# Performance work log

Measured on AMD Instinct MI355X. Metric: run time of the kernel, lower is better.

The kernel has to match this reference:

```python
import jax, jax.numpy as jnp
import numpy as np

N_NODES = 100000
N_EDGES = 3200000
IN_CH = 128
HID = 64
N_CLASSES = 10


def setup_inputs() -> dict:
    key = jax.random.key(0)
    ks = jax.random.split(key, 12)
    def lin(kw, kb, fan_in, fan_out):
        bound = 1.0 / np.sqrt(fan_in)
        W = jax.random.uniform(kw, (fan_in, fan_out), jnp.float32, -bound, bound)
        b = jax.random.uniform(kb, (fan_out,), jnp.float32, -bound, bound)
        return W, b
    x = jax.random.normal(ks[0], (N_NODES, IN_CH), jnp.float32)
    edge_index = jax.random.randint(ks[1], (2, N_EDGES), 0, N_NODES, jnp.int32)
    W1a, b1a = lin(ks[2], ks[3], IN_CH, HID)
    W2a, b2a = lin(ks[4], ks[5], HID, HID)
    W1b, b1b = lin(ks[6], ks[7], HID, HID)
    W2b, b2b = lin(ks[8], ks[9], HID, HID)
    Wl, bl = lin(ks[10], ks[11], HID, N_CLASSES)
    return {"x": x, "edge_index": edge_index,
            "W1a": W1a, "b1a": b1a, "W2a": W2a, "b2a": b2a,
            "W1b": W1b, "b1b": b1b, "W2b": W2b, "b2b": b2b,
            "Wl": Wl, "bl": bl}


def gin_conv(x, src, dst, W1, b1, W2, b2):
    # sum-aggregate neighbor messages: agg[i] = sum_{(src->i)} x[src]
    agg = jax.ops.segment_sum(x[src], dst, num_segments=N_NODES)
    h = agg + x  # (1 + eps) * x with eps = 0 (GINConv default)
    h = jnp.maximum(h @ W1 + b1, 0.0)  # Linear -> ReLU
    return h @ W2 + b2                 # Linear


def reference(x, edge_index, W1a, b1a, W2a, b2a, W1b, b1b, W2b, b2b, Wl, bl):
    src, dst = edge_index[0], edge_index[1]
    h = gin_conv(x, src, dst, W1a, b1a, W2a, b2a)
    h = jnp.maximum(h, 0.0)
    h = gin_conv(h, src, dst, W1b, b1b, W2b, b2b)
    h = jnp.maximum(h, 0.0)
    logits = h @ Wl + bl
    return jax.nn.log_softmax(logits, axis=1)
```

## Files before the change

### kernel.cpp

```cpp
#include <hip/hip_runtime.h>
#include <hip/hip_bf16.h>

#define N_NODES 100000
#define N_EDGES 3200000
#define IN_CH 128
#define HID 64
#define N_CLASSES 10
#define NTILES 6250

#define NB 391
#define NPB 256
#define BCAP 10240
#define CHUNK 8192

typedef unsigned short u16;
typedef unsigned int u32;

typedef __attribute__((ext_vector_type(8))) short bf16x8;
typedef __attribute__((ext_vector_type(4))) float f32x4;

static __device__ __forceinline__ float u2f(u32 u) {
    union { u32 i; float f; } v; v.i = u; return v.f;
}
static __device__ __forceinline__ u16 f2bf(float f) {
    __hip_bfloat16 b = __float2bfloat16(f);
    return *(u16*)&b;
}
static __device__ __forceinline__ u32 pack2(float lo, float hi) {
    return (u32)f2bf(lo) | ((u32)f2bf(hi) << 16);
}


__global__ void __launch_bounds__(1024) passA_k(
        const int* __restrict__ src, const int* __restrict__ dst,
        int* __restrict__ bcnt, u32* __restrict__ stage) {
    __shared__ int lh[NB];
    __shared__ int lb[NB];
    for (int i = threadIdx.x; i < NB; i += 1024) lh[i] = 0;
    __syncthreads();
    int e0 = blockIdx.x * CHUNK;
#pragma unroll
    for (int k = 0; k < CHUNK / 1024; ++k) {
        int e = e0 + k * 1024 + threadIdx.x;
        if (e < N_EDGES) atomicAdd(&lh[dst[e] >> 8], 1);
    }
    __syncthreads();
    for (int i = threadIdx.x; i < NB; i += 1024) {
        lb[i] = atomicAdd(&bcnt[i], lh[i]);
        lh[i] = 0;
    }
    __syncthreads();
#pragma unroll
    for (int k = 0; k < CHUNK / 1024; ++k) {
        int e = e0 + k * 1024 + threadIdx.x;
        if (e < N_EDGES) {
            int d = dst[e];
            int b = d >> 8;
            int p = lb[b] + atomicAdd(&lh[b], 1);
            if (p < BCAP) stage[(size_t)b * BCAP + p] = ((u32)src[e] << 8) | (u32)(d & 255);
        }
    }
}


__global__ void bscan_k(const int* __restrict__ bcnt, int* __restrict__ bbase,
                        int* __restrict__ off) {
    __shared__ int s[512];
    int tid = threadIdx.x;
    int v = (tid < NB) ? min(bcnt[tid], BCAP) : 0;
    s[tid] = v;
    __syncthreads();
    for (int o = 1; o < 512; o <<= 1) {
        int t = (tid >= o) ? s[tid - o] : 0;
        __syncthreads();
        s[tid] += t;
        __syncthreads();
    }
    if (tid < NB) bbase[tid] = s[tid] - v;
    if (tid == NB - 1) off[N_NODES] = s[tid];
}


__global__ void __launch_bounds__(1024) passB_k(
        const int* __restrict__ bcnt, const int* __restrict__ bbase,
        const u32* __restrict__ stage, int* __restrict__ off,
        int* __restrict__ csr) {
    __shared__ int ldeg[NPB];
    __shared__ int loff[NPB + 1];
    __shared__ int lcur[NPB];
    __shared__ int img[BCAP];
    int b = blockIdx.x;
    int nb = min(bcnt[b], BCAP);
    int base = bbase[b];
    const u32* st = stage + (size_t)b * BCAP;
    int tid = threadIdx.x;
    if (tid < NPB) ldeg[tid] = 0;
    __syncthreads();
    for (int i = tid; i < nb; i += 1024) atomicAdd(&ldeg[st[i] & 255u], 1);
    __syncthreads();
    if (tid < NPB) lcur[tid] = ldeg[tid];
    __syncthreads();
    for (int o = 1; o < NPB; o <<= 1) {
        int t = (tid < NPB && tid >= o) ? lcur[tid - o] : 0;
        __syncthreads();
        if (tid < NPB) lcur[tid] += t;
        __syncthreads();
    }
    if (tid < NPB) loff[tid + 1] = lcur[tid];
    if (tid == 0) loff[0] = 0;
    __syncthreads();
    if (tid < NPB) {
        int gnode = (b << 8) + tid;
        if (gnode < N_NODES) off[gnode] = base + loff[tid];
        lcur[tid] = loff[tid];
    }
    __syncthreads();
    for (int i = tid; i < nb; i += 1024) {
        u32 pr = st[i];
        int p = atomicAdd(&lcur[pr & 255u], 1);
        img[p] = (int)(pr >> 8);
    }
    __syncthreads();
    for (int i = tid; i < nb; i += 1024) csr[base + i] = img[i];
}


__global__ void __launch_bounds__(512) gather_k(
        const u16* __restrict__ tab, const int* __restrict__ off,
        const int* __restrict__ csr, u16* __restrict__ outb) {
    int wid = threadIdx.x >> 6, lane = threadIdx.x & 63;
    int g = lane >> 3, c = lane & 7;
    int coff = c << 4;
    const char* tb = (const char*)tab;
    int gw = blockIdx.x * 8 + wid;
    const int NW = 1024 * 8;
    for (int n = gw; n < N_NODES; n += NW) {
        float a0, a1, a2, a3, a4, a5, a6, a7;
        {
            uint4 dS = *(const uint4*)(tb + (size_t)n * 128 + coff);
            u32 sm = (g == 0) ? 0xffffffffu : 0u;
            dS.x &= sm; dS.y &= sm; dS.z &= sm; dS.w &= sm;
            a0 = u2f(dS.x << 16); a1 = u2f(dS.x & 0xffff0000u);
            a2 = u2f(dS.y << 16); a3 = u2f(dS.y & 0xffff0000u);
            a4 = u2f(dS.z << 16); a5 = u2f(dS.z & 0xffff0000u);
            a6 = u2f(dS.w << 16); a7 = u2f(dS.w & 0xffff0000u);
        }
        int e = off[n], e1 = off[n + 1];
        int nfull = (e1 - e) >> 3;
#pragma unroll 4
        for (int it = 0; it < nfull; ++it) {
            int s = csr[e + g];
            uint4 d = *(const uint4*)(tb + (size_t)s * 128 + coff);
            a0 += u2f(d.x << 16); a1 += u2f(d.x & 0xffff0000u);
            a2 += u2f(d.y << 16); a3 += u2f(d.y & 0xffff0000u);
            a4 += u2f(d.z << 16); a5 += u2f(d.z & 0xffff0000u);
            a6 += u2f(d.w << 16); a7 += u2f(d.w & 0xffff0000u);
            e += 8;
        }
        int rem = e1 - e;
        if (rem > 0) {
            int s = csr[e + min(g, rem - 1)];
            u32 m = (g < rem) ? 0xffffffffu : 0u;
            uint4 d = *(const uint4*)(tb + (size_t)s * 128 + coff);
            d.x &= m; d.y &= m; d.z &= m; d.w &= m;
            a0 += u2f(d.x << 16); a1 += u2f(d.x & 0xffff0000u);
            a2 += u2f(d.y << 16); a3 += u2f(d.y & 0xffff0000u);
            a4 += u2f(d.z << 16); a5 += u2f(d.z & 0xffff0000u);
            a6 += u2f(d.w << 16); a7 += u2f(d.w & 0xffff0000u);
        }
        a0 += __shfl_xor(a0, 8);  a1 += __shfl_xor(a1, 8);  a2 += __shfl_xor(a2, 8);
        a3 += __shfl_xor(a3, 8);  a4 += __shfl_xor(a4, 8);  a5 += __shfl_xor(a5, 8);
        a6 += __shfl_xor(a6, 8);  a7 += __shfl_xor(a7, 8);
        a0 += __shfl_xor(a0, 16); a1 += __shfl_xor(a1, 16); a2 += __shfl_xor(a2, 16);
        a3 += __shfl_xor(a3, 16); a4 += __shfl_xor(a4, 16); a5 += __shfl_xor(a5, 16);
        a6 += __shfl_xor(a6, 16); a7 += __shfl_xor(a7, 16);
        a0 += __shfl_xor(a0, 32); a1 += __shfl_xor(a1, 32); a2 += __shfl_xor(a2, 32);
        a3 += __shfl_xor(a3, 32); a4 += __shfl_xor(a4, 32); a5 += __shfl_xor(a5, 32);
        a6 += __shfl_xor(a6, 32); a7 += __shfl_xor(a7, 32);
        if (g == 0) {
            uint4 pk = make_uint4(pack2(a0, a1), pack2(a2, a3), pack2(a4, a5), pack2(a6, a7));
            *(uint4*)((char*)outb + (size_t)n * 128 + coff) = pk;
        }
    }
}


static __device__ __forceinline__ bf16x8 bfragW(const float* __restrict__ W, int ncols,
                                                int kk, int nt, int lane) {
    int k0 = kk * 32 + ((lane >> 4) << 3);
    int col = nt * 16 + (lane & 15);
    bf16x8 b;
#pragma unroll
    for (int j = 0; j < 8; ++j) b[j] = (short)f2bf(W[(size_t)(k0 + j) * ncols + col]);
    return b;
}

static __device__ __forceinline__ bf16x8 bfragWl(const float* __restrict__ Wl,
                                                 int kk, int lane) {
    int k0 = kk * 32 + ((lane >> 4) << 3);
    int col = lane & 15;
    bf16x8 b;
#pragma unroll
    for (int j = 0; j < 8; ++j)
        b[j] = (col < N_CLASSES) ? (short)f2bf(Wl[(size_t)(k0 + j) * N_CLASSES + col]) : (short)0;
    return b;
}

static __device__ __forceinline__ bf16x8 afragSt(const u16* __restrict__ stw,
                                                 int kk, int lane) {
    const u16* p = stw + (size_t)(lane & 15) * 68 + kk * 32 + ((lane >> 4) << 3);
    uint2 q0 = *(const uint2*)p;
    uint2 q1 = *(const uint2*)(p + 4);
    union { uint2 u[2]; bf16x8 v; } cv;
    cv.u[0] = q0; cv.u[1] = q1;
    return cv.v;
}


__global__ void __launch_bounds__(512) lin1_k(
        const float* __restrict__ x, const float* __restrict__ W1,
        u16* __restrict__ yb) {
    __shared__ u16 st[8][16][68];
    int wid = threadIdx.x >> 6, lane = threadIdx.x & 63;
    bf16x8 B[4][4];
#pragma unroll
    for (int kk = 0; kk < 4; ++kk)
#pragma unroll
        for (int nt = 0; nt < 4; ++nt) B[kk][nt] = bfragW(W1, 64, kk, nt, lane);
    int gw = blockIdx.x * 8 + wid;
    const int NW = 782 * 8;
    for (int t = gw; t < NTILES; t += NW) {
        int n0 = t << 4;
        f32x4 acc0 = {0.f, 0.f, 0.f, 0.f}, acc1 = acc0, acc2 = acc0, acc3 = acc0;
#pragma unroll
        for (int kk = 0; kk < 4; ++kk) {
            const float* xr = x + (size_t)(n0 + (lane & 15)) * IN_CH + kk * 32 + ((lane >> 4) << 3);
            float4 f0 = *(const float4*)xr;
            float4 f1 = *(const float4*)(xr + 4);
            bf16x8 a;
            a[0] = (short)f2bf(f0.x); a[1] = (short)f2bf(f0.y);
            a[2] = (short)f2bf(f0.z); a[3] = (short)f2bf(f0.w);
            a[4] = (short)f2bf(f1.x); a[5] = (short)f2bf(f1.y);
            a[6] = (short)f2bf(f1.z); a[7] = (short)f2bf(f1.w);
            acc0 = __builtin_amdgcn_mfma_f32_16x16x32_bf16(a, B[kk][0], acc0, 0, 0, 0);
            acc1 = __builtin_amdgcn_mfma_f32_16x16x32_bf16(a, B[kk][1], acc1, 0, 0, 0);
            acc2 = __builtin_amdgcn_mfma_f32_16x16x32_bf16(a, B[kk][2], acc2, 0, 0, 0);
            acc3 = __builtin_amdgcn_mfma_f32_16x16x32_bf16(a, B[kk][3], acc3, 0, 0, 0);
        }
        int r0 = (lane >> 4) << 2, cl = lane & 15;
#pragma unroll
        for (int i = 0; i < 4; ++i) {
            st[wid][r0 + i][cl]      = f2bf(acc0[i]);
            st[wid][r0 + i][16 + cl] = f2bf(acc1[i]);
            st[wid][r0 + i][32 + cl] = f2bf(acc2[i]);
            st[wid][r0 + i][48 + cl] = f2bf(acc3[i]);
        }
        __builtin_amdgcn_wave_barrier();
        {
            int row = lane >> 2, seg = lane & 3;
            const u16* sp = &st[wid][row][seg * 16];
            uint2 q0 = *(const uint2*)sp;
            uint2 q1 = *(const uint2*)(sp + 4);
            uint2 q2 = *(const uint2*)(sp + 8);
            uint2 q3 = *(const uint2*)(sp + 12);
            char* op = (char*)yb + (size_t)(n0 + row) * 128 + seg * 32;
            *(uint4*)op = make_uint4(q0.x, q0.y, q1.x, q1.y);
            *(uint4*)(op + 16) = make_uint4(q2.x, q2.y, q3.x, q3.y);
        }
        __builtin_amdgcn_wave_barrier();
    }
}


__global__ void __launch_bounds__(512) mlpA_k(
        const u16* __restrict__ ga, const float* __restrict__ b1,
        const float* __restrict__ W2, const float* __restrict__ b2,
        u16* __restrict__ h1b) {
    __shared__ u16 st[8][16][68];
    int wid = threadIdx.x >> 6, lane = threadIdx.x & 63;
    bf16x8 B[2][4];
#pragma unroll
    for (int kk = 0; kk < 2; ++kk)
#pragma unroll
        for (int nt = 0; nt < 4; ++nt) B[kk][nt] = bfragW(W2, 64, kk, nt, lane);
    float b1s[2][8];
#pragma unroll
    for (int kk = 0; kk < 2; ++kk)
#pragma unroll
        for (int j = 0; j < 8; ++j) b1s[kk][j] = b1[kk * 32 + ((lane >> 4) << 3) + j];
    float b2s[4];
#pragma unroll
    for (int nt = 0; nt < 4; ++nt) b2s[nt] = b2[nt * 16 + (lane & 15)];
    int gw = blockIdx.x * 8 + wid;
    const int NW = 782 * 8;
    for (int t = gw; t < NTILES; t += NW) {
        int n0 = t << 4;
        f32x4 acc0 = {0.f, 0.f, 0.f, 0.f}, acc1 = acc0, acc2 = acc0, acc3 = acc0;
#pragma unroll
        for (int kk = 0; kk < 2; ++kk) {
            uint4 raw = *(const uint4*)((const char*)ga + (size_t)(n0 + (lane & 15)) * 128
                                        + kk * 64 + ((lane >> 4) << 4));
            bf16x8 a;
            u32 w0 = raw.x, w1 = raw.y, w2 = raw.z, w3 = raw.w;
            a[0] = (short)f2bf(fmaxf(u2f(w0 << 16) + b1s[kk][0], 0.f));
            a[1] = (short)f2bf(fmaxf(u2f(w0 & 0xffff0000u) + b1s[kk][1], 0.f));
            a[2] = (short)f2bf(fmaxf(u2f(w1 << 16) + b1s[kk][2], 0.f));
            a[3] = (short)f2bf(fmaxf(u2f(w1 & 0xffff0000u) + b1s[kk][3], 0.f));
            a[4] = (short)f2bf(fmaxf(u2f(w2 << 16) + b1s[kk][4], 0.f));
            a[5] = (short)f2bf(fmaxf(u2f(w2 & 0xffff0000u) + b1s[kk][5], 0.f));
            a[6] = (short)f2bf(fmaxf(u2f(w3 << 16) + b1s[kk][6], 0.f));
            a[7] = (short)f2bf(fmaxf(u2f(w3 & 0xffff0000u) + b1s[kk][7], 0.f));
            acc0 = __builtin_amdgcn_mfma_f32_16x16x32_bf16(a, B[kk][0], acc0, 0, 0, 0);
            acc1 = __builtin_amdgcn_mfma_f32_16x16x32_bf16(a, B[kk][1], acc1, 0, 0, 0);
            acc2 = __builtin_amdgcn_mfma_f32_16x16x32_bf16(a, B[kk][2], acc2, 0, 0, 0);
            acc3 = __builtin_amdgcn_mfma_f32_16x16x32_bf16(a, B[kk][3], acc3, 0, 0, 0);
        }
        int r0 = (lane >> 4) << 2, cl = lane & 15;
#pragma unroll
        for (int i = 0; i < 4; ++i) {
            st[wid][r0 + i][cl]      = f2bf(fmaxf(acc0[i] + b2s[0], 0.f));
            st[wid][r0 + i][16 + cl] = f2bf(fmaxf(acc1[i] + b2s[1], 0.f));
            st[wid][r0 + i][32 + cl] = f2bf(fmaxf(acc2[i] + b2s[2], 0.f));
            st[wid][r0 + i][48 + cl] = f2bf(fmaxf(acc3[i] + b2s[3], 0.f));
        }
        __builtin_amdgcn_wave_barrier();
        {
            int row = lane >> 2, seg = lane & 3;
            const u16* sp = &st[wid][row][seg * 16];
            uint2 q0 = *(const uint2*)sp;
            uint2 q1 = *(const uint2*)(sp + 4);
            uint2 q2 = *(const uint2*)(sp + 8);
            uint2 q3 = *(const uint2*)(sp + 12);
            char* op = (char*)h1b + (size_t)(n0 + row) * 128 + seg * 32;
            *(uint4*)op = make_uint4(q0.x, q0.y, q1.x, q1.y);
            *(uint4*)(op + 16) = make_uint4(q2.x, q2.y, q3.x, q3.y);
        }
        __builtin_amdgcn_wave_barrier();
    }
}


__global__ void __launch_bounds__(512) mlpBcls_k(
        const u16* __restrict__ gb, const float* __restrict__ W1,
        const float* __restrict__ b1, const float* __restrict__ W2,
        const float* __restrict__ b2, const float* __restrict__ Wl,
        const float* __restrict__ bl, float* __restrict__ out) {
    __shared__ u16 st[8][16][68];
    int wid = threadIdx.x >> 6, lane = threadIdx.x & 63;
    bf16x8 B1[2][4], B2[2][4], B3[2];
#pragma unroll
    for (int kk = 0; kk < 2; ++kk) {
#pragma unroll
        for (int nt = 0; nt < 4; ++nt) {
            B1[kk][nt] = bfragW(W1, 64, kk, nt, lane);
            B2[kk][nt] = bfragW(W2, 64, kk, nt, lane);
        }
        B3[kk] = bfragWl(Wl, kk, lane);
    }
    int cl = lane & 15;
    float b1s[4], b2s[4];
#pragma unroll
    for (int nt = 0; nt < 4; ++nt) { b1s[nt] = b1[nt * 16 + cl]; b2s[nt] = b2[nt * 16 + cl]; }
    float bls = (cl < N_CLASSES) ? bl[cl] : -1.0e30f;
    int gw = blockIdx.x * 8 + wid;
    const int NW = 782 * 8;
    for (int t = gw; t < NTILES; t += NW) {
        int n0 = t << 4;
        int r0 = (lane >> 4) << 2;
        f32x4 acc0 = {0.f, 0.f, 0.f, 0.f}, acc1 = acc0, acc2 = acc0, acc3 = acc0;
#pragma unroll
        for (int kk = 0; kk < 2; ++kk) {
            bf16x8 a = *(const bf16x8*)((const char*)gb + (size_t)(n0 + cl) * 128
                                        + kk * 64 + ((lane >> 4) << 4));
            acc0 = __builtin_amdgcn_mfma_f32_16x16x32_bf16(a, B1[kk][0], acc0, 0, 0, 0);
            acc1 = __builtin_amdgcn_mfma_f32_16x16x32_bf16(a, B1[kk][1], acc1, 0, 0, 0);
            acc2 = __builtin_amdgcn_mfma_f32_16x16x32_bf16(a, B1[kk][2], acc2, 0, 0, 0);
            acc3 = __builtin_amdgcn_mfma_f32_16x16x32_bf16(a, B1[kk][3], acc3, 0, 0, 0);
        }
#pragma unroll
        for (int i = 0; i < 4; ++i) {
            st[wid][r0 + i][cl]      = f2bf(fmaxf(acc0[i] + b1s[0], 0.f));
            st[wid][r0 + i][16 + cl] = f2bf(fmaxf(acc1[i] + b1s[1], 0.f));
            st[wid][r0 + i][32 + cl] = f2bf(fmaxf(acc2[i] + b1s[2], 0.f));
            st[wid][r0 + i][48 + cl] = f2bf(fmaxf(acc3[i] + b1s[3], 0.f));
        }
        __builtin_amdgcn_wave_barrier();
        f32x4 d0 = {0.f, 0.f, 0.f, 0.f}, d1 = d0, d2 = d0, d3 = d0;
#pragma unroll
        for (int kk = 0; kk < 2; ++kk) {
            bf16x8 a = afragSt(&st[wid][0][0], kk, lane);
            d0 = __builtin_amdgcn_mfma_f32_16x16x32_bf16(a, B2[kk][0], d0, 0, 0, 0);
            d1 = __builtin_amdgcn_mfma_f32_16x16x32_bf16(a, B2[kk][1], d1, 0, 0, 0);
            d2 = __builtin_amdgcn_mfma_f32_16x16x32_bf16(a, B2[kk][2], d2, 0, 0, 0);
            d3 = __builtin_amdgcn_mfma_f32_16x16x32_bf16(a, B2[kk][3], d3, 0, 0, 0);
        }
        __builtin_amdgcn_wave_barrier();
#pragma unroll
        for (int i = 0; i < 4; ++i) {
            st[wid][r0 + i][cl]      = f2bf(fmaxf(d0[i] + b2s[0], 0.f));
            st[wid][r0 + i][16 + cl] = f2bf(fmaxf(d1[i] + b2s[1], 0.f));
            st[wid][r0 + i][32 + cl] = f2bf(fmaxf(d2[i] + b2s[2], 0.f));
            st[wid][r0 + i][48 + cl] = f2bf(fmaxf(d3[i] + b2s[3], 0.f));
        }
        __builtin_amdgcn_wave_barrier();
        f32x4 lg = {0.f, 0.f, 0.f, 0.f};
#pragma unroll
        for (int kk = 0; kk < 2; ++kk) {
            bf16x8 a = afragSt(&st[wid][0][0], kk, lane);
            lg = __builtin_amdgcn_mfma_f32_16x16x32_bf16(a, B3[kk], lg, 0, 0, 0);
        }
        __builtin_amdgcn_wave_barrier();
#pragma unroll
        for (int i = 0; i < 4; ++i) {
            float logit = lg[i] + bls;
            float m = logit;
            m = fmaxf(m, __shfl_xor(m, 1, 16));
            m = fmaxf(m, __shfl_xor(m, 2, 16));
            m = fmaxf(m, __shfl_xor(m, 4, 16));
            m = fmaxf(m, __shfl_xor(m, 8, 16));
            float ex = __expf(logit - m);
            float s = ex;
            s += __shfl_xor(s, 1, 16);
            s += __shfl_xor(s, 2, 16);
            s += __shfl_xor(s, 4, 16);
            s += __shfl_xor(s, 8, 16);
            float ls = __logf(s);
            if (cl < N_CLASSES)
                out[(size_t)(n0 + r0 + i) * N_CLASSES + cl] = logit - m - ls;
        }
    }
}


extern "C" void kernel_launch(void* const* d_in, const int* in_sizes, int n_in,
                              void* d_out, int out_size, void* d_ws, size_t ws_size,
                              hipStream_t stream) {
    const float* x   = (const float*)d_in[0];
    const int*   ei  = (const int*)d_in[1];
    const int*   src = ei;
    const int*   dst = ei + N_EDGES;
    const float* W1a = (const float*)d_in[2];
    const float* b1a = (const float*)d_in[3];
    const float* W2a = (const float*)d_in[4];
    const float* b2a = (const float*)d_in[5];
    const float* W1b = (const float*)d_in[6];
    const float* b1b = (const float*)d_in[7];
    const float* W2b = (const float*)d_in[8];
    const float* b2b = (const float*)d_in[9];
    const float* Wl  = (const float*)d_in[10];
    const float* bl  = (const float*)d_in[11];
    float* out = (float*)d_out;

    char* ws = (char*)d_ws;
    size_t o = 0;
    auto alloc = [&](size_t bytes) -> void* {
        o = (o + 255) & ~(size_t)255;
        void* p = ws + o;
        o += bytes;
        return p;
    };
    int* bcnt  = (int*)alloc((size_t)NB * 4);
    int* bbase = (int*)alloc((size_t)NB * 4);
    int* off   = (int*)alloc((size_t)(N_NODES + 1) * 4);
    u32* stage = (u32*)alloc((size_t)NB * BCAP * 4);
    int* csr   = (int*)alloc((size_t)N_EDGES * 4);
    u16* yb    = (u16*)alloc((size_t)N_NODES * 64 * 2);
    u16* ga    = (u16*)alloc((size_t)N_NODES * 64 * 2);
    u16* h1b   = (u16*)alloc((size_t)N_NODES * 64 * 2);
    u16* gb    = (u16*)alloc((size_t)N_NODES * 64 * 2);

    hipMemsetAsync(bcnt, 0, (size_t)NB * 4, stream);

    const int nA = (N_EDGES + CHUNK - 1) / CHUNK;
    passA_k<<<nA, 1024, 0, stream>>>(src, dst, bcnt, stage);
    bscan_k<<<1, 512, 0, stream>>>(bcnt, bbase, off);
    passB_k<<<NB, 1024, 0, stream>>>(bcnt, bbase, stage, off, csr);

    lin1_k   <<<782, 512, 0, stream>>>(x, W1a, yb);
    gather_k <<<1024, 512, 0, stream>>>(yb, off, csr, ga);
    mlpA_k   <<<782, 512, 0, stream>>>(ga, b1a, W2a, b2a, h1b);
    gather_k <<<1024, 512, 0, stream>>>(h1b, off, csr, gb);
    mlpBcls_k<<<782, 512, 0, stream>>>(gb, W1b, b1b, W2b, b2b, Wl, bl, out);
}
```

Measured before the change: 323.8 us.

## Fuse neighbor gathers into MLP kernels and fold bucket scan into passB

The standalone gather kernels are removed and the neighbor aggregation is done directly inside the MLP kernels. Each lane gathers one node of a 16-node tile and keeps fp32 accumulators, so the aggregated bf16 intermediates no longer round-trip through global memory. The separate single-block bucket scan is recomputed redundantly in every passB block to save a launch, and weight fragments are staged through shared memory instead of registers. The trade-off is that the gather now runs one node per lane with divergent edge loops and fewer waves in flight, which may reduce memory-level parallelism for the irregular loads.

After: 371.3 us. 14.7% more time.

```diff
diff --git a/kernel.cpp b/kernel.cpp
--- a/kernel.cpp
+++ b/kernel.cpp
@@ -25,9 +25,6 @@
 static __device__ __forceinline__ u16 f2bf(float f) {
     __hip_bfloat16 b = __float2bfloat16(f);
     return *(u16*)&b;
-}
-static __device__ __forceinline__ u32 pack2(float lo, float hi) {
-    return (u32)f2bf(lo) | ((u32)f2bf(hi) << 16);
 }
 
 
@@ -63,37 +60,28 @@
 }
 
 
-__global__ void bscan_k(const int* __restrict__ bcnt, int* __restrict__ bbase,
-                        int* __restrict__ off) {
-    __shared__ int s[512];
-    int tid = threadIdx.x;
-    int v = (tid < NB) ? min(bcnt[tid], BCAP) : 0;
-    s[tid] = v;
-    __syncthreads();
-    for (int o = 1; o < 512; o <<= 1) {
-        int t = (tid >= o) ? s[tid - o] : 0;
-        __syncthreads();
-        s[tid] += t;
-        __syncthreads();
-    }
-    if (tid < NB) bbase[tid] = s[tid] - v;
-    if (tid == NB - 1) off[N_NODES] = s[tid];
-}
-
-
 __global__ void __launch_bounds__(1024) passB_k(
-        const int* __restrict__ bcnt, const int* __restrict__ bbase,
-        const u32* __restrict__ stage, int* __restrict__ off,
-        int* __restrict__ csr) {
+        const int* __restrict__ bcnt, const u32* __restrict__ stage,
+        int* __restrict__ off, int* __restrict__ csr) {
+    __shared__ int sc[512];
     __shared__ int ldeg[NPB];
     __shared__ int loff[NPB + 1];
     __shared__ int lcur[NPB];
     __shared__ int img[BCAP];
     int b = blockIdx.x;
+    int tid = threadIdx.x;
+    if (tid < 512) sc[tid] = (tid < NB) ? min(bcnt[tid], BCAP) : 0;
+    __syncthreads();
+    for (int o = 1; o < 512; o <<= 1) {
+        int t = (tid < 512 && tid >= o) ? sc[tid - o] : 0;
+        __syncthreads();
+        if (tid < 512) sc[tid] += t;
+        __syncthreads();
+    }
+    int base = (b == 0) ? 0 : sc[b - 1];
+    if (b == 0 && tid == 0) off[N_NODES] = sc[NB - 1];
     int nb = min(bcnt[b], BCAP);
-    int base = bbase[b];
     const u32* st = stage + (size_t)b * BCAP;
-    int tid = threadIdx.x;
     if (tid < NPB) ldeg[tid] = 0;
     __syncthreads();
     for (int i = tid; i < nb; i += 1024) atomicAdd(&ldeg[st[i] & 255u], 1);
@@ -122,66 +110,6 @@
     }
     __syncthreads();
     for (int i = tid; i < nb; i += 1024) csr[base + i] = img[i];
-}
-
-
-__global__ void __launch_bounds__(512) gather_k(
-        const u16* __restrict__ tab, const int* __restrict__ off,
-        const int* __restrict__ csr, u16* __restrict__ outb) {
-    int wid = threadIdx.x >> 6, lane = threadIdx.x & 63;
-    int g = lane >> 3, c = lane & 7;
-    int coff = c << 4;
-    const char* tb = (const char*)tab;
-    int gw = blockIdx.x * 8 + wid;
-    const int NW = 1024 * 8;
-    for (int n = gw; n < N_NODES; n += NW) {
-        float a0, a1, a2, a3, a4, a5, a6, a7;
-        {
-            uint4 dS = *(const uint4*)(tb + (size_t)n * 128 + coff);
-            u32 sm = (g == 0) ? 0xffffffffu : 0u;
-            dS.x &= sm; dS.y &= sm; dS.z &= sm; dS.w &= sm;
-            a0 = u2f(dS.x << 16); a1 = u2f(dS.x & 0xffff0000u);
-            a2 = u2f(dS.y << 16); a3 = u2f(dS.y & 0xffff0000u);
-            a4 = u2f(dS.z << 16); a5 = u2f(dS.z & 0xffff0000u);
-            a6 = u2f(dS.w << 16); a7 = u2f(dS.w & 0xffff0000u);
-        }
-        int e = off[n], e1 = off[n + 1];
-        int nfull = (e1 - e) >> 3;
-#pragma unroll 4
-        for (int it = 0; it < nfull; ++it) {
-            int s = csr[e + g];
-            uint4 d = *(const uint4*)(tb + (size_t)s * 128 + coff);
-            a0 += u2f(d.x << 16); a1 += u2f(d.x & 0xffff0000u);
-            a2 += u2f(d.y << 16); a3 += u2f(d.y & 0xffff0000u);
-            a4 += u2f(d.z << 16); a5 += u2f(d.z & 0xffff0000u);
-            a6 += u2f(d.w << 16); a7 += u2f(d.w & 0xffff0000u);
-            e += 8;
-        }
-        int rem = e1 - e;
-        if (rem > 0) {
-            int s = csr[e + min(g, rem - 1)];
-            u32 m = (g < rem) ? 0xffffffffu : 0u;
-            uint4 d = *(const uint4*)(tb + (size_t)s * 128 + coff);
-            d.x &= m; d.y &= m; d.z &= m; d.w &= m;
-            a0 += u2f(d.x << 16); a1 += u2f(d.x & 0xffff0000u);
-            a2 += u2f(d.y << 16); a3 += u2f(d.y & 0xffff0000u);
-            a4 += u2f(d.z << 16); a5 += u2f(d.z & 0xffff0000u);
-            a6 += u2f(d.w << 16); a7 += u2f(d.w & 0xffff0000u);
-        }
-        a0 += __shfl_xor(a0, 8);  a1 += __shfl_xor(a1, 8);  a2 += __shfl_xor(a2, 8);
-        a3 += __shfl_xor(a3, 8);  a4 += __shfl_xor(a4, 8);  a5 += __shfl_xor(a5, 8);
-        a6 += __shfl_xor(a6, 8);  a7 += __shfl_xor(a7, 8);
-        a0 += __shfl_xor(a0, 16); a1 += __shfl_xor(a1, 16); a2 += __shfl_xor(a2, 16);
-        a3 += __shfl_xor(a3, 16); a4 += __shfl_xor(a4, 16); a5 += __shfl_xor(a5, 16);
-        a6 += __shfl_xor(a6, 16); a7 += __shfl_xor(a7, 16);
-        a0 += __shfl_xor(a0, 32); a1 += __shfl_xor(a1, 32); a2 += __shfl_xor(a2, 32);
-        a3 += __shfl_xor(a3, 32); a4 += __shfl_xor(a4, 32); a5 += __shfl_xor(a5, 32);
-        a6 += __shfl_xor(a6, 32); a7 += __shfl_xor(a7, 32);
-        if (g == 0) {
-            uint4 pk = make_uint4(pack2(a0, a1), pack2(a2, a3), pack2(a4, a5), pack2(a6, a7));
-            *(uint4*)((char*)outb + (size_t)n * 128 + coff) = pk;
-        }
-    }
 }
 
 
@@ -215,6 +143,47 @@
     cv.u[0] = q0; cv.u[1] = q1;
     return cv.v;
 }
+
+#define ACC8(acc, c)                                                   \
+    acc[0] += u2f(c.x << 16); acc[1] += u2f(c.x & 0xffff0000u);        \
+    acc[2] += u2f(c.y << 16); acc[3] += u2f(c.y & 0xffff0000u);        \
+    acc[4] += u2f(c.z << 16); acc[5] += u2f(c.z & 0xffff0000u);        \
+    acc[6] += u2f(c.w << 16); acc[7] += u2f(c.w & 0xffff0000u);
+
+#define GATHER16(TAB)                                                  \
+    int node = n0 + (lane & 15);                                       \
+    int q4 = (lane >> 4) << 4;                                         \
+    const char* tb = (const char*)(TAB);                               \
+    float accA[8], accB[8];                                            \
+    {   const char* rp = tb + (size_t)node * 128 + q4;                 \
+        uint4 c0 = *(const uint4*)rp;                                  \
+        uint4 c1 = *(const uint4*)(rp + 64);                           \
+        accA[0] = u2f(c0.x << 16); accA[1] = u2f(c0.x & 0xffff0000u);  \
+        accA[2] = u2f(c0.y << 16); accA[3] = u2f(c0.y & 0xffff0000u);  \
+        accA[4] = u2f(c0.z << 16); accA[5] = u2f(c0.z & 0xffff0000u);  \
+        accA[6] = u2f(c0.w << 16); accA[7] = u2f(c0.w & 0xffff0000u);  \
+        accB[0] = u2f(c1.x << 16); accB[1] = u2f(c1.x & 0xffff0000u);  \
+        accB[2] = u2f(c1.y << 16); accB[3] = u2f(c1.y & 0xffff0000u);  \
+        accB[4] = u2f(c1.z << 16); accB[5] = u2f(c1.z & 0xffff0000u);  \
+        accB[6] = u2f(c1.w << 16); accB[7] = u2f(c1.w & 0xffff0000u); }\
+    int e = off[node], e1 = off[node + 1];                             \
+    while (__ballot(e < e1)) {                                         \
+        if (e < e1) {                                                  \
+            int s = csr[e];                                            \
+            const char* rp = tb + (size_t)s * 128 + q4;                \
+            uint4 c0 = *(const uint4*)rp;                              \
+            uint4 c1 = *(const uint4*)(rp + 64);                       \
+            ACC8(accA, c0) ACC8(accB, c1)                              \
+        }                                                              \
+        if (e + 1 < e1) {                                              \
+            int s = csr[e + 1];                                        \
+            const char* rp = tb + (size_t)s * 128 + q4;                \
+            uint4 c0 = *(const uint4*)rp;                              \
+            uint4 c1 = *(const uint4*)(rp + 64);                       \
+            ACC8(accA, c0) ACC8(accB, c1)                              \
+        }                                                              \
+        e += 2;                                                        \
+    }
 
 
 __global__ void __launch_bounds__(512) lin1_k(
@@ -272,91 +241,86 @@
 }
 
 
-__global__ void __launch_bounds__(512) mlpA_k(
-        const u16* __restrict__ ga, const float* __restrict__ b1,
+__global__ void __launch_bounds__(512) gfA_k(
+        const u16* __restrict__ yb, const int* __restrict__ off,
+        const int* __restrict__ csr, const float* __restrict__ b1,
         const float* __restrict__ W2, const float* __restrict__ b2,
         u16* __restrict__ h1b) {
+    __shared__ u16 sWf[8][64][8];
     __shared__ u16 st[8][16][68];
     int wid = threadIdx.x >> 6, lane = threadIdx.x & 63;
-    bf16x8 B[2][4];
-#pragma unroll
-    for (int kk = 0; kk < 2; ++kk)
-#pragma unroll
-        for (int nt = 0; nt < 4; ++nt) B[kk][nt] = bfragW(W2, 64, kk, nt, lane);
-    float b1s[2][8];
-#pragma unroll
-    for (int kk = 0; kk < 2; ++kk)
-#pragma unroll
-        for (int j = 0; j < 8; ++j) b1s[kk][j] = b1[kk * 32 + ((lane >> 4) << 3) + j];
+    for (int f = wid; f < 8; f += 8)
+        *(bf16x8*)&sWf[f][lane][0] = bfragW(W2, 64, f >> 2, f & 3, lane);
+    __syncthreads();
+    int qq = (lane >> 4) << 3, cl = lane & 15;
+    float b1A[8], b1B[8];
+#pragma unroll
+    for (int j = 0; j < 8; ++j) { b1A[j] = b1[qq + j]; b1B[j] = b1[32 + qq + j]; }
     float b2s[4];
 #pragma unroll
-    for (int nt = 0; nt < 4; ++nt) b2s[nt] = b2[nt * 16 + (lane & 15)];
+    for (int nt = 0; nt < 4; ++nt) b2s[nt] = b2[nt * 16 + cl];
     int gw = blockIdx.x * 8 + wid;
     const int NW = 782 * 8;
     for (int t = gw; t < NTILES; t += NW) {
         int n0 = t << 4;
-        f32x4 acc0 = {0.f, 0.f, 0.f, 0.f}, acc1 = acc0, acc2 = acc0, acc3 = acc0;
-#pragma unroll
-        for (int kk = 0; kk < 2; ++kk) {
-            uint4 raw = *(const uint4*)((const char*)ga + (size_t)(n0 + (lane & 15)) * 128
-                                        + kk * 64 + ((lane >> 4) << 4));
-            bf16x8 a;
-            u32 w0 = raw.x, w1 = raw.y, w2 = raw.z, w3 = raw.w;
-            a[0] = (short)f2bf(fmaxf(u2f(w0 << 16) + b1s[kk][0], 0.f));
-            a[1] = (short)f2bf(fmaxf(u2f(w0 & 0xffff0000u) + b1s[kk][1], 0.f));
-            a[2] = (short)f2bf(fmaxf(u2f(w1 << 16) + b1s[kk][2], 0.f));
-            a[3] = (short)f2bf(fmaxf(u2f(w1 & 0xffff0000u) + b1s[kk][3], 0.f));
-            a[4] = (short)f2bf(fmaxf(u2f(w2 << 16) + b1s[kk][4], 0.f));
-            a[5] = (short)f2bf(fmaxf(u2f(w2 & 0xffff0000u) + b1s[kk][5], 0.f));
-            a[6] = (short)f2bf(fmaxf(u2f(w3 << 16) + b1s[kk][6], 0.f));
-            a[7] = (short)f2bf(fmaxf(u2f(w3 & 0xffff0000u) + b1s[kk][7], 0.f));
-            acc0 = __builtin_amdgcn_mfma_f32_16x16x32_bf16(a, B[kk][0], acc0, 0, 0, 0);
-            acc1 = __builtin_amdgcn_mfma_f32_16x16x32_bf16(a, B[kk][1], acc1, 0, 0, 0);
-            acc2 = __builtin_amdgcn_mfma_f32_16x16x32_bf16(a, B[kk][2], acc2, 0, 0, 0);
-            acc3 = __builtin_amdgcn_mfma_f32_16x16x32_bf16(a, B[kk][3], acc3, 0, 0, 0);
-        }
-        int r0 = (lane >> 4) << 2, cl = lane & 15;
+        GATHER16(yb)
+        bf16x8 a0, a1;
+#pragma unroll
+        for (int j = 0; j < 8; ++j) {
+            a0[j] = (short)f2bf(fmaxf(accA[j] + b1A[j], 0.f));
+            a1[j] = (short)f2bf(fmaxf(accB[j] + b1B[j], 0.f));
+        }
+        f32x4 d0 = {0.f, 0.f, 0.f, 0.f}, d1 = d0, d2 = d0, d3 = d0;
+        d0 = __builtin_amdgcn_mfma_f32_16x16x32_bf16(a0, *(const bf16x8*)&sWf[0][lane][0], d0, 0, 0, 0);
+        d1 = __builtin_amdgcn_mfma_f32_16x16x32_bf16(a0, *(const bf16x8*)&sWf[1][lane][0], d1, 0, 0, 0);
+        d2 = __builtin_amdgcn_mfma_f32_16x16x32_bf16(a0, *(const bf16x8*)&sWf[2][lane][0], d2, 0, 0, 0);
+        d3 = __builtin_amdgcn_mfma_f32_16x16x32_bf16(a0, *(const bf16x8*)&sWf[3][lane][0], d3, 0, 0, 0);
+        d0 = __builtin_amdgcn_mfma_f32_16x16x32_bf16(a1, *(const bf16x8*)&sWf[4][lane][0], d0, 0, 0, 0);
+        d1 = __builtin_amdgcn_mfma_f32_16x16x32_bf16(a1, *(const bf16x8*)&sWf[5][lane][0], d1, 0, 0, 0);
+        d2 = __builtin_amdgcn_mfma_f32_16x16x32_bf16(a1, *(const bf16x8*)&sWf[6][lane][0], d2, 0, 0, 0);
+        d3 = __builtin_amdgcn_mfma_f32_16x16x32_bf16(a1, *(const bf16x8*)&sWf[7][lane][0], d3, 0, 0, 0);
+        int r0 = (lane >> 4) << 2;
 #pragma unroll
         for (int i = 0; i < 4; ++i) {
-            st[wid][r0 + i][cl]      = f2bf(fmaxf(acc0[i] + b2s[0], 0.f));
-            st[wid][r0 + i][16 + cl] = f2bf(fmaxf(acc1[i] + b2s[1], 0.f));
-            st[wid][r0 + i][32 + cl] = f2bf(fmaxf(acc2[i] + b2s[2], 0.f));
-            st[wid][r0 + i][48 + cl] = f2bf(fmaxf(acc3[i] + b2s[3], 0.f));
+            st[wid][r0 + i][cl]      = f2bf(fmaxf(d0[i] + b2s[0], 0.f));
+            st[wid][r0 + i][16 + cl] = f2bf(fmaxf(d1[i] + b2s[1], 0.f));
+            st[wid][r0 + i][32 + cl] = f2bf(fmaxf(d2[i] + b2s[2], 0.f));
+            st[wid][r0 + i][48 + cl] = f2bf(fmaxf(d3[i] + b2s[3], 0.f));
         }
         __builtin_amdgcn_wave_barrier();
         {
             int row = lane >> 2, seg = lane & 3;
             const u16* sp = &st[wid][row][seg * 16];
-            uint2 q0 = *(const uint2*)sp;
-            uint2 q1 = *(const uint2*)(sp + 4);
-            uint2 q2 = *(const uint2*)(sp + 8);
-            uint2 q3 = *(const uint2*)(sp + 12);
+            uint2 w0 = *(const uint2*)sp;
+            uint2 w1 = *(const uint2*)(sp + 4);
+            uint2 w2 = *(const uint2*)(sp + 8);
+            uint2 w3 = *(const uint2*)(sp + 12);
             char* op = (char*)h1b + (size_t)(n0 + row) * 128 + seg * 32;
-            *(uint4*)op = make_uint4(q0.x, q0.y, q1.x, q1.y);
-            *(uint4*)(op + 16) = make_uint4(q2.x, q2.y, q3.x, q3.y);
-        }
-        __builtin_amdgcn_wave_barrier();
-    }
-}
-
-
-__global__ void __launch_bounds__(512) mlpBcls_k(
-        const u16* __restrict__ gb, const float* __restrict__ W1,
+            *(uint4*)op = make_uint4(w0.x, w0.y, w1.x, w1.y);
+            *(uint4*)(op + 16) = make_uint4(w2.x, w2.y, w3.x, w3.y);
+        }
+        __builtin_amdgcn_wave_barrier();
+    }
+}
+
+
+__global__ void __launch_bounds__(512) gfB_k(
+        const u16* __restrict__ h1b, const int* __restrict__ off,
+        const int* __restrict__ csr, const float* __restrict__ W1,
         const float* __restrict__ b1, const float* __restrict__ W2,
         const float* __restrict__ b2, const float* __restrict__ Wl,
         const float* __restrict__ bl, float* __restrict__ out) {
+    __shared__ u16 sWf[18][64][8];
     __shared__ u16 st[8][16][68];
     int wid = threadIdx.x >> 6, lane = threadIdx.x & 63;
-    bf16x8 B1[2][4], B2[2][4], B3[2];
-#pragma unroll
-    for (int kk = 0; kk < 2; ++kk) {
-#pragma unroll
-        for (int nt = 0; nt < 4; ++nt) {
-            B1[kk][nt] = bfragW(W1, 64, kk, nt, lane);
-            B2[kk][nt] = bfragW(W2, 64, kk, nt, lane);
-        }
-        B3[kk] = bfragWl(Wl, kk, lane);
-    }
+    for (int f = wid; f < 18; f += 8) {
+        bf16x8 v;
+        if (f < 8)       v = bfragW(W1, 64, f >> 2, f & 3, lane);
+        else if (f < 16) v = bfragW(W2, 64, (f - 8) >> 2, (f - 8) & 3, lane);
+        else             v = bfragWl(Wl, f - 16, lane);
+        *(bf16x8*)&sWf[f][lane][0] = v;
+    }
+    __syncthreads();
     int cl = lane & 15;
     float b1s[4], b2s[4];
 #pragma unroll
@@ -366,33 +330,39 @@
     const int NW = 782 * 8;
     for (int t = gw; t < NTILES; t += NW) {
         int n0 = t << 4;
+        GATHER16(h1b)
+        bf16x8 a0, a1;
+#pragma unroll
+        for (int j = 0; j < 8; ++j) {
+            a0[j] = (short)f2bf(accA[j]);
+            a1[j] = (short)f2bf(accB[j]);
+        }
+        f32x4 u0 = {0.f, 0.f, 0.f, 0.f}, u1 = u0, u2 = u0, u3 = u0;
+        u0 = __builtin_amdgcn_mfma_f32_16x16x32_bf16(a0, *(const bf16x8*)&sWf[0][lane][0], u0, 0, 0, 0);
+        u1 = __builtin_amdgcn_mfma_f32_16x16x32_bf16(a0, *(const bf16x8*)&sWf[1][lane][0], u1, 0, 0, 0);
+        u2 = __builtin_amdgcn_mfma_f32_16x16x32_bf16(a0, *(const bf16x8*)&sWf[2][lane][0], u2, 0, 0, 0);
+        u3 = __builtin_amdgcn_mfma_f32_16x16x32_bf16(a0, *(const bf16x8*)&sWf[3][lane][0], u3, 0, 0, 0);
+        u0 = __builtin_amdgcn_mfma_f32_16x16x32_bf16(a1, *(const bf16x8*)&sWf[4][lane][0], u0, 0, 0, 0);
+        u1 = __builtin_amdgcn_mfma_f32_16x16x32_bf16(a1, *(const bf16x8*)&sWf[5][lane][0], u1, 0, 0, 0);
+        u2 = __builtin_amdgcn_mfma_f32_16x16x32_bf16(a1, *(const bf16x8*)&sWf[6][lane][0], u2, 0, 0, 0);
+        u3 = __builtin_amdgcn_mfma_f32_16x16x32_bf16(a1, *(const bf16x8*)&sWf[7][lane][0], u3, 0, 0, 0);
         int r0 = (lane >> 4) << 2;
-        f32x4 acc0 = {0.f, 0.f, 0.f, 0.f}, acc1 = acc0, acc2 = acc0, acc3 = acc0;
-#pragma unroll
-        for (int kk = 0; kk < 2; ++kk) {
-            bf16x8 a = *(const bf16x8*)((const char*)gb + (size_t)(n0 + cl) * 128
-                                        + kk * 64 + ((lane >> 4) << 4));
-            acc0 = __builtin_amdgcn_mfma_f32_16x16x32_bf16(a, B1[kk][0], acc0, 0, 0, 0);
-            acc1 = __builtin_amdgcn_mfma_f32_16x16x32_bf16(a, B1[kk][1], acc1, 0, 0, 0);
-            acc2 = __builtin_amdgcn_mfma_f32_16x16x32_bf16(a, B1[kk][2], acc2, 0, 0, 0);
-            acc3 = __builtin_amdgcn_mfma_f32_16x16x32_bf16(a, B1[kk][3], acc3, 0, 0, 0);
-        }
 #pragma unroll
         for (int i = 0; i < 4; ++i) {
-            st[wid][r0 + i][cl]      = f2bf(fmaxf(acc0[i] + b1s[0], 0.f));
-            st[wid][r0 + i][16 + cl] = f2bf(fmaxf(acc1[i] + b1s[1], 0.f));
-            st[wid][r0 + i][32 + cl] = f2bf(fmaxf(acc2[i] + b1s[2], 0.f));
-            st[wid][r0 + i][48 + cl] = f2bf(fmaxf(acc3[i] + b1s[3], 0.f));
+            st[wid][r0 + i][cl]      = f2bf(fmaxf(u0[i] + b1s[0], 0.f));
+            st[wid][r0 + i][16 + cl] = f2bf(fmaxf(u1[i] + b1s[1], 0.f));
+            st[wid][r0 + i][32 + cl] = f2bf(fmaxf(u2[i] + b1s[2], 0.f));
+            st[wid][r0 + i][48 + cl] = f2bf(fmaxf(u3[i] + b1s[3], 0.f));
         }
         __builtin_amdgcn_wave_barrier();
         f32x4 d0 = {0.f, 0.f, 0.f, 0.f}, d1 = d0, d2 = d0, d3 = d0;
 #pragma unroll
         for (int kk = 0; kk < 2; ++kk) {
             bf16x8 a = afragSt(&st[wid][0][0], kk, lane);
-            d0 = __builtin_amdgcn_mfma_f32_16x16x32_bf16(a, B2[kk][0], d0, 0, 0, 0);
-            d1 = __builtin_amdgcn_mfma_f32_16x16x32_bf16(a, B2[kk][1], d1, 0, 0, 0);
-            d2 = __builtin_amdgcn_mfma_f32_16x16x32_bf16(a, B2[kk][2], d2, 0, 0, 0);
-            d3 = __builtin_amdgcn_mfma_f32_16x16x32_bf16(a, B2[kk][3], d3, 0, 0, 0);
+            d0 = __builtin_amdgcn_mfma_f32_16x16x32_bf16(a, *(const bf16x8*)&sWf[8 + kk * 4 + 0][lane][0], d0, 0, 0, 0);
+            d1 = __builtin_amdgcn_mfma_f32_16x16x32_bf16(a, *(const bf16x8*)&sWf[8 + kk * 4 + 1][lane][0], d1, 0, 0, 0);
+            d2 = __builtin_amdgcn_mfma_f32_16x16x32_bf16(a, *(const bf16x8*)&sWf[8 + kk * 4 + 2][lane][0], d2, 0, 0, 0);
+            d3 = __builtin_amdgcn_mfma_f32_16x16x32_bf16(a, *(const bf16x8*)&sWf[8 + kk * 4 + 3][lane][0], d3, 0, 0, 0);
         }
         __builtin_amdgcn_wave_barrier();
 #pragma unroll
@@ -407,7 +377,7 @@
 #pragma unroll
         for (int kk = 0; kk < 2; ++kk) {
             bf16x8 a = afragSt(&st[wid][0][0], kk, lane);
-            lg = __builtin_amdgcn_mfma_f32_16x16x32_bf16(a, B3[kk], lg, 0, 0, 0);
+            lg = __builtin_amdgcn_mfma_f32_16x16x32_bf16(a, *(const bf16x8*)&sWf[16 + kk][lane][0], lg, 0, 0, 0);
         }
         __builtin_amdgcn_wave_barrier();
 #pragma unroll
@@ -460,25 +430,19 @@
         return p;
     };
     int* bcnt  = (int*)alloc((size_t)NB * 4);
-    int* bbase = (int*)alloc((size_t)NB * 4);
     int* off   = (int*)alloc((size_t)(N_NODES + 1) * 4);
     u32* stage = (u32*)alloc((size_t)NB * BCAP * 4);
     int* csr   = (int*)alloc((size_t)N_EDGES * 4);
     u16* yb    = (u16*)alloc((size_t)N_NODES * 64 * 2);
-    u16* ga    = (u16*)alloc((size_t)N_NODES * 64 * 2);
     u16* h1b   = (u16*)alloc((size_t)N_NODES * 64 * 2);
-    u16* gb    = (u16*)alloc((size_t)N_NODES * 64 * 2);
 
     hipMemsetAsync(bcnt, 0, (size_t)NB * 4, stream);
 
     const int nA = (N_EDGES + CHUNK - 1) / CHUNK;
     passA_k<<<nA, 1024, 0, stream>>>(src, dst, bcnt, stage);
-    bscan_k<<<1, 512, 0, stream>>>(bcnt, bbase, off);
-    passB_k<<<NB, 1024, 0, stream>>>(bcnt, bbase, stage, off, csr);
-
-    lin1_k   <<<782, 512, 0, stream>>>(x, W1a, yb);
-    gather_k <<<1024, 512, 0, stream>>>(yb, off, csr, ga);
-    mlpA_k   <<<782, 512, 0, stream>>>(ga, b1a, W2a, b2a, h1b);
-    gather_k <<<1024, 512, 0, stream>>>(h1b, off, csr, gb);
-    mlpBcls_k<<<782, 512, 0, stream>>>(gb, W1b, b1b, W2b, b2b, Wl, bl, out);
-}
+    passB_k<<<NB, 1024, 0, stream>>>(bcnt, stage, off, csr);
+
+    lin1_k<<<782, 512, 0, stream>>>(x, W1a, yb);
+    gfA_k <<<782, 512, 0, stream>>>(yb, off, csr, b1a, W2a, b2a, h1b);
+    gfB_k <<<782, 512, 0, stream>>>(h1b, off, csr, W1b, b1b, W2b, b2b, Wl, bl, out);
+}
```
